# Performance work log

Hardware: AMD Instinct MI355X
Metric: run time of the kernel (lower is better)

The kernel has to match this reference:

```python
import jax, jax.numpy as jnp
import numpy as np
from jax import lax

EPS = 1e-5

def setup_inputs() -> dict:
    key = jax.random.key(0)
    ks = jax.random.split(key, 8)
    B, D, H, W = 2, 96, 96, 96
    K, N, R = 4, 16, 6
    return {
        "x": jax.random.normal(ks[0], (B, D, H, W), jnp.float32),
        "x_proj_weight": jax.random.normal(ks[1], (K, R + 2 * N, D), jnp.float32) * 0.05,
        "dt_projs_weight": jax.random.normal(ks[2], (K, D, R), jnp.float32) * 0.05,
        "dt_projs_bias": jax.random.normal(ks[3], (K, D), jnp.float32) * 0.05,
        "A_logs": jax.random.uniform(ks[4], (K * D, N), jnp.float32, 0.0, 1.0),
        "Ds": jax.random.normal(ks[5], (K * D,), jnp.float32) * 0.1,
        "norm_weight": jnp.ones((D,), jnp.float32),
        "norm_bias": jnp.zeros((D,), jnp.float32),
    }

def _cross_scan(x):
    # x: [B,C,H,W] -> xs: [B,4,C,L]; dirs: row-major, col-major, and their flips
    B, C, H, W = x.shape
    x_hw = x.reshape(B, C, H * W)
    x_wh = jnp.swapaxes(x, 2, 3).reshape(B, C, H * W)
    return jnp.stack([x_hw, x_wh, x_hw[..., ::-1], x_wh[..., ::-1]], axis=1)

def _cross_merge(ys, H, W):
    # ys: [B,4,C,L] -> y: [B,C,L]
    B, K, C, L = ys.shape
    ys = ys[:, 0:2] + ys[:, 2:4][..., ::-1]
    y_wh = jnp.swapaxes(ys[:, 1].reshape(B, C, W, H), 2, 3).reshape(B, C, L)
    return ys[:, 0] + y_wh

def _forward(x, x_proj_weight, dt_projs_weight, dt_projs_bias, A_logs, Ds,
             norm_weight, norm_bias):
    B, D, H, W = x.shape
    L = H * W
    K, _, R = dt_projs_weight.shape
    N = A_logs.shape[1]

    xs = _cross_scan(x)                                        # [B,K,D,L]
    x_dbl = jnp.einsum('bkdl,kcd->bkcl', xs, x_proj_weight)    # [B,K,R+2N,L]
    dts, Bs, Cs = x_dbl[:, :, :R], x_dbl[:, :, R:R + N], x_dbl[:, :, R + N:]
    dts = jnp.einsum('bkrl,kdr->bkdl', dts, dt_projs_weight)   # [B,K,D,L]

    A = -jnp.exp(A_logs).reshape(K, D, N)                      # [K,D,N]
    delta = jax.nn.softplus(dts + dt_projs_bias[None, :, :, None])  # [B,K,D,L]

    # time-major for scan
    u_t = jnp.moveaxis(xs, 3, 0)       # [L,B,K,D]
    d_t = jnp.moveaxis(delta, 3, 0)    # [L,B,K,D]
    B_t = jnp.moveaxis(Bs, 3, 0)       # [L,B,K,N]
    C_t = jnp.moveaxis(Cs, 3, 0)       # [L,B,K,N]

    def step(h, inp):
        u, dlt, b, c = inp
        h = jnp.exp(dlt[..., None] * A) * h + (dlt * u)[..., None] * b[:, :, None, :]
        y = jnp.einsum('bkdn,bkn->bkd', h, c)
        return h, y

    h0 = jnp.zeros((B, K, D, N), xs.dtype)
    _, ys = lax.scan(step, h0, (u_t, d_t, B_t, C_t))           # ys: [L,B,K,D]
    ys = jnp.moveaxis(ys, 0, 3)                                # [B,K,D,L]
    ys = ys + Ds.reshape(1, K, D, 1) * xs                      # skip term

    y = _cross_merge(ys, H, W)                                 # [B,D,L]
    y = jnp.swapaxes(y, 1, 2)                                  # [B,L,D]
    # out_norm: LayerNorm over channel dim
    mu = y.mean(-1, keepdims=True)
    var = y.var(-1, keepdims=True)
    y = (y - mu) / jnp.sqrt(var + EPS) * norm_weight + norm_bias
    return y.reshape(B, H, W, D)

def reference(x, x_proj_weight, dt_projs_weight, dt_projs_bias, A_logs, Ds,
              norm_weight, norm_bias):
    return _forward(x, x_proj_weight, dt_projs_weight, dt_projs_bias,
                    A_logs, Ds, norm_weight, norm_bias)
```

## Files before the change

kernel.cpp:

```cpp
#include <hip/hip_runtime.h>
#include <hip/hip_bf16.h>
#include <hip/hip_fp16.h>


constexpr int Bn = 2, Kn = 4, Dn = 96, Hn = 96, Wn = 96, Ln = Hn * Wn;
constexpr int Nn = 16, Rn = 6;
constexpr int CCn = 144, CLn = 64;

#define DI __device__ __forceinline__

typedef _Float16 half2v __attribute__((ext_vector_type(2)));

DI float bf2f(unsigned short u) { return __uint_as_float(((unsigned)u) << 16); }
DI bool probe_bf16(const void* nw) { return ((const unsigned*)nw)[0] == 0x3F803F80u; }
DI float ld_in(const void* p, long i, bool bf) {
  return bf ? bf2f(((const unsigned short*)p)[i]) : ((const float*)p)[i];
}
DI float fexp2(float x) {
#if __has_builtin(__builtin_amdgcn_exp2f)
  return __builtin_amdgcn_exp2f(x);
#else
  return exp2f(x);
#endif
}
DI float softplus_fast(float v) {
  return (v > 15.f) ? v : __logf(1.f + __expf(v));
}
DI float dot2acc(unsigned a, unsigned b, float c) {
#if __has_builtin(__builtin_amdgcn_fdot2)
  half2v av, bv;
  __builtin_memcpy(&av, &a, 4);
  __builtin_memcpy(&bv, &b, 4);
  return __builtin_amdgcn_fdot2(av, bv, c, false);
#else
  __half2 ah = *(__half2*)&a, bh = *(__half2*)&b;
  float2 af = __half22float2(ah), bf2_ = __half22float2(bh);
  return fmaf(af.y, bf2_.y, fmaf(af.x, bf2_.x, c));
#endif
}
DI float quad_reduce_add(float v) {
  int a = __builtin_amdgcn_mov_dpp(__float_as_int(v), 0xB1, 0xF, 0xF, true);
  v += __int_as_float(a);
  int b = __builtin_amdgcn_mov_dpp(__float_as_int(v), 0x4E, 0xF, 0xF, true);
  v += __int_as_float(b);
  return v;
}
constexpr float LOG2E = 1.44269504088896340736f;

__global__ __launch_bounds__(256) void k_prep(
    const void* __restrict__ x, const void* __restrict__ xpw,
    const void* __restrict__ dtw, const void* __restrict__ dtb,
    const void* __restrict__ Al, const void* __restrict__ Ds,
    const void* __restrict__ nw, const void* __restrict__ nb,
    float* __restrict__ xl, float* __restrict__ xlT,
    float* __restrict__ wp_f, float* __restrict__ wdt_f,
    float* __restrict__ bias_f, float* __restrict__ Al_f,
    float* __restrict__ dsum, float* __restrict__ nw_f, float* __restrict__ nb_f) {
  __shared__ float tile[96 * 97];
  bool bf = probe_bf16(nw);
  int h = blockIdx.x, b = blockIdx.y;
  int tid = threadIdx.x;
  int fi = (blockIdx.y * gridDim.x + blockIdx.x) * 256 + tid;
  int fgs = gridDim.x * gridDim.y * 256;
  for (int i = fi; i < Kn * 38 * Dn; i += fgs) wp_f[i] = ld_in(xpw, i, bf);
  for (int i = fi; i < Kn * Dn * Rn; i += fgs) wdt_f[i] = ld_in(dtw, i, bf);
  for (int i = fi; i < Kn * Dn; i += fgs) bias_f[i] = ld_in(dtb, i, bf);
  for (int i = fi; i < Kn * Dn * Nn; i += fgs)
    Al_f[i] = -__expf(ld_in(Al, i, bf)) * LOG2E;
  for (int i = fi; i < Dn; i += fgs) {
    dsum[i] = ld_in(Ds, i, bf) + ld_in(Ds, 96 + i, bf) +
              ld_in(Ds, 192 + i, bf) + ld_in(Ds, 288 + i, bf);
    nw_f[i] = ld_in(nw, i, bf);
    nb_f[i] = ld_in(nb, i, bf);
  }
  long srcbase = (long)b * Dn * Ln + (long)h * 96;
  for (int i = tid; i < 96 * 96; i += 256) {
    int d = i / 96, w = i - d * 96;
    tile[d * 97 + w] = ld_in(x, srcbase + (long)d * Ln + w, bf);
  }
  __syncthreads();
  float* xlb = xl + (size_t)b * Ln * 96;
  float* xTb = xlT + (size_t)b * Ln * 96;
  for (int i = tid; i < 96 * 96; i += 256) {
    int w = i / 96, d = i - w * 96;
    float v = tile[d * 97 + w];
    xlb[(size_t)(h * 96 + w) * 96 + d] = v;
    xTb[(size_t)(w * 96 + h) * 96 + d] = v;
  }
}

__global__ __launch_bounds__(256) void k_proj(
    const float* __restrict__ xl, const float* __restrict__ xlT,
    const float* __restrict__ wp_f, const float* __restrict__ wdt_f,
    const float* __restrict__ bias_f, const float* __restrict__ Al_f,
    __half2* __restrict__ ddu, __half* __restrict__ BCh,
    float* __restrict__ PSg) {
  constexpr int TL = 64;
  __shared__ __half xt[TL * 102];
  __shared__ __half wp[40 * 100];
  __shared__ __half xd2[TL * 40];
  __shared__ unsigned wdt_u[96 * 4];
  __shared__ float bias[96];
  int tile = blockIdx.x, k = blockIdx.y, b = blockIdx.z;
  int l0 = tile * TL;
  int tid = threadIdx.x;
  bool rev = (k & 2) != 0;

  for (int i = tid; i < 40 * 100; i += 256) {
    int c = i / 100, dd = i - c * 100;
    wp[i] = __float2half((c < 38 && dd < 96) ? wp_f[k * 38 * 96 + c * 96 + dd]
                                             : 0.f);
  }
  for (int i = tid; i < 96 * 3; i += 256) {
    int d = i / 3, rr = i - d * 3;
    __half2 hv = __floats2half2_rn(wdt_f[k * 576 + d * 6 + rr * 2],
                                   wdt_f[k * 576 + d * 6 + rr * 2 + 1]);
    wdt_u[d * 4 + rr] = *(unsigned*)&hv;
  }
  if (tid < 96) bias[tid] = bias_f[k * 96 + tid];
  {
    const float* xsrc = ((k & 1) ? xlT : xl) + (size_t)b * Ln * 96;
    for (int i = tid; i < TL * 24; i += 256) {
      int r = i / 24, q = i - r * 24;
      int g = rev ? (Ln - 1 - l0 - r) : (l0 + r);
      float4 v = *(const float4*)(xsrc + (size_t)g * 96 + q * 4);
      *(__half2*)(&xt[r * 102 + q * 4]) = __floats2half2_rn(v.x, v.y);
      *(__half2*)(&xt[r * 102 + q * 4 + 2]) = __floats2half2_rn(v.z, v.w);
    }
  }
  __syncthreads();

  {
    int jg = tid & 31, cg = tid >> 5;
    int j0 = jg * 2, c0 = cg * 5;
    float acc[5][2];
#pragma unroll
    for (int i = 0; i < 5; ++i) { acc[i][0] = 0.f; acc[i][1] = 0.f; }
    for (int dd = 0; dd < 96; dd += 4) {
      uint2 xa = *(const uint2*)&xt[(j0 + 0) * 102 + dd];
      uint2 xb = *(const uint2*)&xt[(j0 + 1) * 102 + dd];
#pragma unroll
      for (int i = 0; i < 5; ++i) {
        uint2 wv = *(const uint2*)&wp[(c0 + i) * 100 + dd];
        acc[i][0] = dot2acc(xa.x, wv.x, acc[i][0]);
        acc[i][0] = dot2acc(xa.y, wv.y, acc[i][0]);
        acc[i][1] = dot2acc(xb.x, wv.x, acc[i][1]);
        acc[i][1] = dot2acc(xb.y, wv.y, acc[i][1]);
      }
    }
#pragma unroll
    for (int i = 0; i < 5; ++i) {
      xd2[j0 * 40 + c0 + i] = __float2half(acc[i][0]);
      xd2[(j0 + 1) * 40 + c0 + i] = __float2half(acc[i][1]);
    }
  }
  __syncthreads();

  size_t bk = (size_t)b * 4 + k;
  {
    __half2* o = (__half2*)(BCh + (bk * (size_t)Ln + l0) * 32);
    for (int i = tid; i < TL * 16; i += 256) {
      int j = i >> 4, cp = i & 15;
      int c = cp * 2;
      int ng = c >> 3, idx = c & 7;
      int ch = (idx < 4) ? (6 + ng * 4 + idx) : (22 + ng * 4 + (idx - 4));
      o[i] = *(const __half2*)&xd2[j * 40 + ch];
    }
  }
  if (tid < 192) {
    int d = tid >> 1, hg = tid & 1;
    unsigned wv0 = wdt_u[d * 4], wv1 = wdt_u[d * 4 + 1], wv2 = wdt_u[d * 4 + 2];
    float bd = bias[d];
    float ac2[8];
    *(float4*)&ac2[0] = *(const float4*)&Al_f[(k * 96 + d) * 16 + hg * 8];
    *(float4*)&ac2[4] = *(const float4*)&Al_f[(k * 96 + d) * 16 + hg * 8 + 4];
    float P[8] = {1.f, 1.f, 1.f, 1.f, 1.f, 1.f, 1.f, 1.f};
    float S[8] = {0.f, 0.f, 0.f, 0.f, 0.f, 0.f, 0.f, 0.f};
    __half2* dcol = ddu + (bk * (size_t)Ln + l0) * 96 + d;
#pragma unroll 2
    for (int t = 0; t < TL; ++t) {
      uint2 xr01 = *(const uint2*)&xd2[t * 40];
      unsigned xr2 = *(const unsigned*)&xd2[t * 40 + 4];
      float v = dot2acc(xr01.x, wv0,
                dot2acc(xr01.y, wv1,
                dot2acc(xr2, wv2, bd)));
      float sp = softplus_fast(v);
      float u = __half2float(xt[t * 102 + d]);
      __half2 pk = __floats2half2_rn(sp, sp * u);
      if (hg == 0) dcol[(size_t)t * 96] = pk;
      float2 pf = __half22float2(pk);
      float spc = pf.x, fy = pf.y;
#pragma unroll
      for (int w = 0; w < 4; ++w) {
        unsigned bw = *(const unsigned*)&xd2[t * 40 + 6 + 8 * hg + 2 * w];
        float2 Bv = __half22float2(*(__half2*)&bw);
        float a0 = fexp2(spc * ac2[w * 2]);
        P[w * 2] *= a0;
        S[w * 2] = fmaf(a0, S[w * 2], fy * Bv.x);
        float a1 = fexp2(spc * ac2[w * 2 + 1]);
        P[w * 2 + 1] *= a1;
        S[w * 2 + 1] = fmaf(a1, S[w * 2 + 1], fy * Bv.y);
      }
    }
    size_t ob = ((size_t)(bk * 96 + d) * CCn + tile) * 32 + hg * 8;
    *(float4*)&PSg[ob] = make_float4(P[0], P[1], P[2], P[3]);
    *(float4*)&PSg[ob + 4] = make_float4(P[4], P[5], P[6], P[7]);
    *(float4*)&PSg[ob + 16] = make_float4(S[0], S[1], S[2], S[3]);
    *(float4*)&PSg[ob + 20] = make_float4(S[4], S[5], S[6], S[7]);
  }
}

__global__ __launch_bounds__(256) void k_midscan(float* __restrict__ PSg) {
  __shared__ float Pl[256], Sl[256];
  int bkd = blockIdx.x;
  int tid = threadIdx.x;
  int g = tid >> 4, n = tid & 15;
  constexpr int CPG = CCn / 16;
  size_t base = ((size_t)bkd * CCn + (size_t)g * CPG) * 32 + n;
  float Pr[CPG], Sr[CPG];
#pragma unroll
  for (int i = 0; i < CPG; ++i) {
    Pr[i] = PSg[base + (size_t)i * 32];
    Sr[i] = PSg[base + (size_t)i * 32 + 16];
  }
  float Pa = 1.f, Sa = 0.f;
#pragma unroll
  for (int i = 0; i < CPG; ++i) { Sa = fmaf(Pr[i], Sa, Sr[i]); Pa *= Pr[i]; }
  Pl[tid] = Pa;
  Sl[tid] = Sa;
  __syncthreads();
#pragma unroll
  for (int s = 1; s < 16; s <<= 1) {
    float Pp = 1.f, Sp = 0.f;
    if (g >= s) { Pp = Pl[(g - s) * 16 + n]; Sp = Sl[(g - s) * 16 + n]; }
    __syncthreads();
    if (g >= s) {
      Sl[tid] = fmaf(Pl[tid], Sp, Sl[tid]);
      Pl[tid] *= Pp;
    }
    __syncthreads();
  }
  float h = (g == 0) ? 0.f : Sl[(g - 1) * 16 + n];
#pragma unroll
  for (int i = 0; i < CPG; ++i) {
    PSg[base + (size_t)i * 32] = h;
    h = fmaf(Pr[i], h, Sr[i]);
  }
}

__global__ __launch_bounds__(192) void k_scan2(
    const __half2* __restrict__ ddu, const __half* __restrict__ BCh,
    const float* __restrict__ Al_f, const float* __restrict__ PSg,
    __half* __restrict__ ysH) {
  __shared__ __half2 dd_s[CLn * 96];
  __shared__ __half bc_s[CLn * 32];
  int chunk = blockIdx.x, k = blockIdx.y, b = blockIdx.z;
  int tid = threadIdx.x;
  int dp = tid >> 2, ng = tid & 3;
  int d0 = dp * 2, n0 = ng * 4;
  int bk = b * 4 + k;
  int t0 = chunk * CLn;
  float ac[2][4];
#pragma unroll
  for (int dd = 0; dd < 2; ++dd)
#pragma unroll
    for (int j = 0; j < 4; ++j)
      ac[dd][j] = Al_f[(k * 96 + d0 + dd) * 16 + n0 + j];
  {
    const uint4* dsrc = (const uint4*)(ddu + ((size_t)bk * Ln + t0) * 96);
    uint4* ddst = (uint4*)dd_s;
    for (int i = tid; i < CLn * 96 / 4; i += 192) ddst[i] = dsrc[i];
    const uint4* bsrc = (const uint4*)(BCh + ((size_t)bk * Ln + t0) * 32);
    uint4* bdst = (uint4*)bc_s;
    for (int i = tid; i < CLn * 32 * 2 / 16; i += 192) bdst[i] = bsrc[i];
  }
  float4 ha = *(const float4*)(PSg + ((size_t)(bk * 96 + d0) * CCn + chunk) * 32 + n0);
  float4 hb = *(const float4*)(PSg + ((size_t)(bk * 96 + d0 + 1) * CCn + chunk) * 32 + n0);
  float h[2][4] = {{ha.x, ha.y, ha.z, ha.w}, {hb.x, hb.y, hb.z, hb.w}};
  __syncthreads();

#pragma unroll 2
  for (int t = 0; t < CLn; ++t) {
    union { uint2 u; __half2 h2[2]; } dv;
    dv.u = *(const uint2*)&dd_s[t * 96 + d0];
    union { uint4 u; __half2 h2[4]; } bc;
    bc.u = *(const uint4*)&bc_s[t * 32 + ng * 8];
    float2 f0 = __half22float2(dv.h2[0]);
    float2 f1 = __half22float2(dv.h2[1]);
    float2 b01 = __half22float2(bc.h2[0]);
    float2 b23 = __half22float2(bc.h2[1]);
    float2 c01 = __half22float2(bc.h2[2]);
    float2 c23 = __half22float2(bc.h2[3]);
    float Ba[4] = {b01.x, b01.y, b23.x, b23.y};
    float Ca[4] = {c01.x, c01.y, c23.x, c23.y};
    float py0 = 0.f, py1 = 0.f;
#pragma unroll
    for (int j = 0; j < 4; ++j) {
      float a0 = fexp2(f0.x * ac[0][j]);
      h[0][j] = fmaf(a0, h[0][j], f0.y * Ba[j]);
      py0 = fmaf(h[0][j], Ca[j], py0);
      float a1 = fexp2(f1.x * ac[1][j]);
      h[1][j] = fmaf(a1, h[1][j], f1.y * Ba[j]);
      py1 = fmaf(h[1][j], Ca[j], py1);
    }
    py0 = quad_reduce_add(py0);
    py1 = quad_reduce_add(py1);
    if (ng == 0)
      *(__half2*)&ysH[((size_t)bk * Ln + t0 + t) * 96 + d0] =
          __halves2half2(__float2half(py0), __float2half(py1));
  }
}

__global__ __launch_bounds__(256) void k_merge_ln(
    const __half* __restrict__ ysH, const float* __restrict__ xl,
    const float* __restrict__ dsum, const void* __restrict__ nwraw,
    const float* __restrict__ nw_f, const float* __restrict__ nb_f,
    void* __restrict__ outv) {
  __shared__ float yt[64 * 98];
  __shared__ float nwf[96], nbf[96], dsm[96], mu_s[64], rs_s[64];
  bool bf = probe_bf16(nwraw);
  int tile = blockIdx.x, b = blockIdx.y;
  int h0 = (tile / 12) * 8, w0 = (tile % 12) * 8;
  int tid = threadIdx.x;
  if (tid < 96) {
    nwf[tid] = nw_f[tid];
    nbf[tid] = nb_f[tid];
    dsm[tid] = dsum[tid];
  }
  const __half* y0 = ysH + (size_t)(b * 4 + 0) * Ln * 96;
  const __half* y1 = ysH + (size_t)(b * 4 + 1) * Ln * 96;
  const __half* y2 = ysH + (size_t)(b * 4 + 2) * Ln * 96;
  const __half* y3 = ysH + (size_t)(b * 4 + 3) * Ln * 96;
  const float* xb = xl + (size_t)b * Ln * 96;
  __syncthreads();
  for (int i = tid; i < 64 * 48; i += 256) {
    int rr = i / 48, dp = i - rr * 48, d = dp * 2;
    int hh = h0 + (rr >> 3), ww = w0 + (rr & 7);
    int l = hh * 96 + ww, t1 = ww * 96 + hh;
    float2 v0 = __half22float2(*(const __half2*)&y0[(size_t)l * 96 + d]);
    float2 v1 = __half22float2(*(const __half2*)&y1[(size_t)t1 * 96 + d]);
    float2 v2 = __half22float2(*(const __half2*)&y2[(size_t)(Ln - 1 - l) * 96 + d]);
    float2 v3 = __half22float2(*(const __half2*)&y3[(size_t)(Ln - 1 - t1) * 96 + d]);
    float2 xv = *(const float2*)&xb[(size_t)l * 96 + d];
    float2 r;
    r.x = v0.x + v1.x + v2.x + v3.x + dsm[d] * xv.x;
    r.y = v0.y + v1.y + v2.y + v3.y + dsm[d + 1] * xv.y;
    *(float2*)&yt[rr * 98 + d] = r;
  }
  __syncthreads();
  {
    int rr = tid >> 2, qq = tid & 3;
    float s = 0.f, ss = 0.f;
#pragma unroll 4
    for (int d2 = 0; d2 < 24; ++d2) {
      float v = yt[rr * 98 + qq * 24 + d2];
      s += v;
      ss += v * v;
    }
    s = quad_reduce_add(s);
    ss = quad_reduce_add(ss);
    if (qq == 0) {
      float mu = s * (1.f / 96.f);
      float var = fmaxf(ss * (1.f / 96.f) - mu * mu, 0.f);
      mu_s[rr] = mu;
      rs_s[rr] = rsqrtf(var + 1e-5f);
    }
  }
  __syncthreads();
  for (int i = tid; i < 64 * 48; i += 256) {
    int rr = i / 48, dp = i - rr * 48, d = dp * 2;
    int hh = h0 + (rr >> 3), ww = w0 + (rr & 7);
    size_t idx = ((size_t)b * Ln + hh * 96 + ww) * 96 + d;
    float2 yv = *(const float2*)&yt[rr * 98 + d];
    float mu = mu_s[rr], rs = rs_s[rr];
    float o0 = (yv.x - mu) * rs * nwf[d] + nbf[d];
    float o1 = (yv.y - mu) * rs * nwf[d + 1] + nbf[d + 1];
    if (bf) {
      union { unsigned u; unsigned short us[2]; } pk;
      __hip_bfloat16 b0 = __float2bfloat16(o0), b1 = __float2bfloat16(o1);
      pk.us[0] = *(unsigned short*)&b0;
      pk.us[1] = *(unsigned short*)&b1;
      *(unsigned*)&((__hip_bfloat16*)outv)[idx] = pk.u;
    } else {
      *(float2*)&((float*)outv)[idx] = make_float2(o0, o1);
    }
  }
}

extern "C" void kernel_launch(void* const* d_in, const int* in_sizes, int n_in,
                              void* d_out, int out_size, void* d_ws, size_t ws_size,
                              hipStream_t stream) {
  const void* x   = d_in[0];
  const void* xpw = d_in[1];
  const void* dtw = d_in[2];
  const void* dtb = d_in[3];
  const void* Al  = d_in[4];
  const void* Ds  = d_in[5];
  const void* nw  = d_in[6];
  const void* nb  = d_in[7];

  char* ws = (char*)d_ws;
  size_t off = 0;
  auto alloc = [&](size_t bytes) {
    char* p = ws + off;
    off += (bytes + 511) & ~(size_t)511;
    return p;
  };
  float* xl    = (float*)alloc((size_t)Bn * Ln * Dn * 4);
  float* xlT   = (float*)alloc((size_t)Bn * Ln * Dn * 4);
  float* wp_f  = (float*)alloc((size_t)Kn * 38 * Dn * 4);
  float* wdt_f = (float*)alloc((size_t)Kn * Dn * Rn * 4);
  float* bias_f= (float*)alloc((size_t)Kn * Dn * 4);
  float* Al_f  = (float*)alloc((size_t)Kn * Dn * Nn * 4);
  float* dsum  = (float*)alloc((size_t)Dn * 4);
  float* nw_f  = (float*)alloc((size_t)Dn * 4);
  float* nb_f  = (float*)alloc((size_t)Dn * 4);
  __half2* ddu = (__half2*)alloc((size_t)Bn * Kn * Ln * Dn * 4);
  __half* BCh  = (__half*)alloc((size_t)Bn * Kn * Ln * 32 * 2);
  float* PS    = (float*)alloc((size_t)Bn * Kn * Dn * CCn * 32 * 4);
  __half* ysH  = (__half*)alloc((size_t)Bn * Kn * Ln * Dn * 2);
  (void)ws_size; (void)in_sizes; (void)n_in; (void)out_size;

  k_prep<<<dim3(Hn, Bn), dim3(256), 0, stream>>>(
      x, xpw, dtw, dtb, Al, Ds, nw, nb, xl, xlT, wp_f, wdt_f, bias_f, Al_f,
      dsum, nw_f, nb_f);
  k_proj<<<dim3(Ln / 64, Kn, Bn), dim3(256), 0, stream>>>(
      xl, xlT, wp_f, wdt_f, bias_f, Al_f, ddu, BCh, PS);
  k_midscan<<<dim3(Bn * Kn * Dn), dim3(256), 0, stream>>>(PS);
  k_scan2<<<dim3(CCn, Kn, Bn), dim3(192), 0, stream>>>(ddu, BCh, Al_f, PS, ysH);
  k_merge_ln<<<dim3(144, Bn), dim3(256), 0, stream>>>(ysH, xl, dsum, nw, nw_f,
                                                      nb_f, d_out);
}
```

Baseline: 198.7 us.

## Halve scan chunk length and pre-pack fp16 projection weights in prep kernel

Scan chunks shrink from 64 to 32 timesteps, which doubles the chunk count and the number of projection tiles, giving more parallel blocks in the projection and second-pass scan kernels. The projection weights are converted to padded fp16 and packed dt weights once in the prep kernel, so each projection block only does vectorized copies into shared memory instead of per-block conversion. In exchange the chunk-prefix buffer doubles, the mid-scan kernel has twice as many serial chunk-combine steps, and each projection thread now computes one row instead of two, which reduces weight reuse per shared-memory load.

```diff
diff --git a/kernel.cpp b/kernel.cpp
--- a/kernel.cpp
+++ b/kernel.cpp
@@ -5,7 +5,7 @@
 
 constexpr int Bn = 2, Kn = 4, Dn = 96, Hn = 96, Wn = 96, Ln = Hn * Wn;
 constexpr int Nn = 16, Rn = 6;
-constexpr int CCn = 144, CLn = 64;
+constexpr int CCn = 288, CLn = 32;
 
 #define DI __device__ __forceinline__
 
@@ -53,7 +53,7 @@
     const void* __restrict__ Al, const void* __restrict__ Ds,
     const void* __restrict__ nw, const void* __restrict__ nb,
     float* __restrict__ xl, float* __restrict__ xlT,
-    float* __restrict__ wp_f, float* __restrict__ wdt_f,
+    __half* __restrict__ wp_h, unsigned* __restrict__ wdt_p,
     float* __restrict__ bias_f, float* __restrict__ Al_f,
     float* __restrict__ dsum, float* __restrict__ nw_f, float* __restrict__ nb_f) {
   __shared__ float tile[96 * 97];
@@ -62,9 +62,29 @@
   int tid = threadIdx.x;
   int fi = (blockIdx.y * gridDim.x + blockIdx.x) * 256 + tid;
   int fgs = gridDim.x * gridDim.y * 256;
-  for (int i = fi; i < Kn * 38 * Dn; i += fgs) wp_f[i] = ld_in(xpw, i, bf);
-  for (int i = fi; i < Kn * Dn * Rn; i += fgs) wdt_f[i] = ld_in(dtw, i, bf);
-  for (int i = fi; i < Kn * Dn; i += fgs) bias_f[i] = ld_in(dtb, i, bf);
+  for (int i = fi; i < Kn * 4000; i += fgs) {
+    int k = i / 4000, r = i - k * 4000;
+    int c = r / 100, dd = r - c * 100;
+    wp_h[i] = __float2half(
+        (c < 38 && dd < 96) ? ld_in(xpw, (long)k * 38 * 96 + c * 96 + dd, bf)
+                            : 0.f);
+  }
+  for (int i = fi; i < Kn * Dn; i += fgs) {
+    float r01a = ld_in(dtw, (long)i * 6 + 0, bf);
+    float r01b = ld_in(dtw, (long)i * 6 + 1, bf);
+    float r23a = ld_in(dtw, (long)i * 6 + 2, bf);
+    float r23b = ld_in(dtw, (long)i * 6 + 3, bf);
+    float r45a = ld_in(dtw, (long)i * 6 + 4, bf);
+    float r45b = ld_in(dtw, (long)i * 6 + 5, bf);
+    __half2 h01 = __floats2half2_rn(r01a, r01b);
+    __half2 h23 = __floats2half2_rn(r23a, r23b);
+    __half2 h45 = __floats2half2_rn(r45a, r45b);
+    wdt_p[i * 4 + 0] = *(unsigned*)&h01;
+    wdt_p[i * 4 + 1] = *(unsigned*)&h23;
+    wdt_p[i * 4 + 2] = *(unsigned*)&h45;
+    wdt_p[i * 4 + 3] = 0u;
+    bias_f[i] = ld_in(dtb, i, bf);
+  }
   for (int i = fi; i < Kn * Dn * Nn; i += fgs)
     Al_f[i] = -__expf(ld_in(Al, i, bf)) * LOG2E;
   for (int i = fi; i < Dn; i += fgs) {
@@ -91,11 +111,11 @@
 
 __global__ __launch_bounds__(256) void k_proj(
     const float* __restrict__ xl, const float* __restrict__ xlT,
-    const float* __restrict__ wp_f, const float* __restrict__ wdt_f,
+    const __half* __restrict__ wp_h, const unsigned* __restrict__ wdt_p,
     const float* __restrict__ bias_f, const float* __restrict__ Al_f,
     __half2* __restrict__ ddu, __half* __restrict__ BCh,
     float* __restrict__ PSg) {
-  constexpr int TL = 64;
+  constexpr int TL = 32;
   __shared__ __half xt[TL * 102];
   __shared__ __half wp[40 * 100];
   __shared__ __half xd2[TL * 40];
@@ -106,18 +126,13 @@
   int tid = threadIdx.x;
   bool rev = (k & 2) != 0;
 
-  for (int i = tid; i < 40 * 100; i += 256) {
-    int c = i / 100, dd = i - c * 100;
-    wp[i] = __float2half((c < 38 && dd < 96) ? wp_f[k * 38 * 96 + c * 96 + dd]
-                                             : 0.f);
-  }
-  for (int i = tid; i < 96 * 3; i += 256) {
-    int d = i / 3, rr = i - d * 3;
-    __half2 hv = __floats2half2_rn(wdt_f[k * 576 + d * 6 + rr * 2],
-                                   wdt_f[k * 576 + d * 6 + rr * 2 + 1]);
-    wdt_u[d * 4 + rr] = *(unsigned*)&hv;
-  }
-  if (tid < 96) bias[tid] = bias_f[k * 96 + tid];
+  {
+    const uint4* wsrc = (const uint4*)(wp_h + (size_t)k * 4000);
+    for (int i = tid; i < 500; i += 256) ((uint4*)wp)[i] = wsrc[i];
+    const uint4* dsrc = (const uint4*)(wdt_p + (size_t)k * 384);
+    for (int i = tid; i < 96; i += 256) ((uint4*)wdt_u)[i] = dsrc[i];
+    if (tid < 96) bias[tid] = bias_f[k * 96 + tid];
+  }
   {
     const float* xsrc = ((k & 1) ? xlT : xl) + (size_t)b * Ln * 96;
     for (int i = tid; i < TL * 24; i += 256) {
@@ -132,27 +147,19 @@
 
   {
     int jg = tid & 31, cg = tid >> 5;
-    int j0 = jg * 2, c0 = cg * 5;
-    float acc[5][2];
-#pragma unroll
-    for (int i = 0; i < 5; ++i) { acc[i][0] = 0.f; acc[i][1] = 0.f; }
+    int c0 = cg * 5;
+    float acc[5] = {0.f, 0.f, 0.f, 0.f, 0.f};
     for (int dd = 0; dd < 96; dd += 4) {
-      uint2 xa = *(const uint2*)&xt[(j0 + 0) * 102 + dd];
-      uint2 xb = *(const uint2*)&xt[(j0 + 1) * 102 + dd];
+      uint2 xa = *(const uint2*)&xt[jg * 102 + dd];
 #pragma unroll
       for (int i = 0; i < 5; ++i) {
         uint2 wv = *(const uint2*)&wp[(c0 + i) * 100 + dd];
-        acc[i][0] = dot2acc(xa.x, wv.x, acc[i][0]);
-        acc[i][0] = dot2acc(xa.y, wv.y, acc[i][0]);
-        acc[i][1] = dot2acc(xb.x, wv.x, acc[i][1]);
-        acc[i][1] = dot2acc(xb.y, wv.y, acc[i][1]);
+        acc[i] = dot2acc(xa.x, wv.x, acc[i]);
+        acc[i] = dot2acc(xa.y, wv.y, acc[i]);
       }
     }
 #pragma unroll
-    for (int i = 0; i < 5; ++i) {
-      xd2[j0 * 40 + c0 + i] = __float2half(acc[i][0]);
-      xd2[(j0 + 1) * 40 + c0 + i] = __float2half(acc[i][1]);
-    }
+    for (int i = 0; i < 5; ++i) xd2[jg * 40 + c0 + i] = __float2half(acc[i]);
   }
   __syncthreads();
 
@@ -408,8 +415,8 @@
   };
   float* xl    = (float*)alloc((size_t)Bn * Ln * Dn * 4);
   float* xlT   = (float*)alloc((size_t)Bn * Ln * Dn * 4);
-  float* wp_f  = (float*)alloc((size_t)Kn * 38 * Dn * 4);
-  float* wdt_f = (float*)alloc((size_t)Kn * Dn * Rn * 4);
+  __half* wp_h = (__half*)alloc((size_t)Kn * 4000 * 2);
+  unsigned* wdt_p = (unsigned*)alloc((size_t)Kn * Dn * 4 * 4);
   float* bias_f= (float*)alloc((size_t)Kn * Dn * 4);
   float* Al_f  = (float*)alloc((size_t)Kn * Dn * Nn * 4);
   float* dsum  = (float*)alloc((size_t)Dn * 4);
@@ -422,10 +429,10 @@
   (void)ws_size; (void)in_sizes; (void)n_in; (void)out_size;
 
   k_prep<<<dim3(Hn, Bn), dim3(256), 0, stream>>>(
-      x, xpw, dtw, dtb, Al, Ds, nw, nb, xl, xlT, wp_f, wdt_f, bias_f, Al_f,
+      x, xpw, dtw, dtb, Al, Ds, nw, nb, xl, xlT, wp_h, wdt_p, bias_f, Al_f,
       dsum, nw_f, nb_f);
-  k_proj<<<dim3(Ln / 64, Kn, Bn), dim3(256), 0, stream>>>(
-      xl, xlT, wp_f, wdt_f, bias_f, Al_f, ddu, BCh, PS);
+  k_proj<<<dim3(Ln / 32, Kn, Bn), dim3(256), 0, stream>>>(
+      xl, xlT, wp_h, wdt_p, bias_f, Al_f, ddu, BCh, PS);
   k_midscan<<<dim3(Bn * Kn * Dn), dim3(256), 0, stream>>>(PS);
   k_scan2<<<dim3(CCn, Kn, Bn), dim3(192), 0, stream>>>(ddu, BCh, Al_f, PS, ysH);
   k_merge_ln<<<dim3(144, Bn), dim3(256), 0, stream>>>(ysH, xl, dsum, nw, nw_f,
```

After: 184.4 us. 1.08x faster.

## Fuse projection, chunk-carry scan and output scan into one cooperative kernel

Applied to the files above, without the earlier changes.

Merges k_proj, k_midscan and k_scan2 into a single cooperative kernel with grid-wide syncs. Projected B/C and delta stay in shared memory across the phases instead of round-tripping ddu/BCh through global memory. It also precomputes fp16 weights in k_prep and replaces the per-step P product with one exp2 of the summed delta. This adds dependence on a cooperative launch of 1152 blocks fitting co-resident (occupancy hint of 5), falls back to the split path if the launch fails, and pays for grid-sync overhead.

```diff
diff --git a/kernel.cpp b/kernel.cpp
--- a/kernel.cpp
+++ b/kernel.cpp
@@ -1,11 +1,14 @@
 #include <hip/hip_runtime.h>
 #include <hip/hip_bf16.h>
 #include <hip/hip_fp16.h>
-
+#include <hip/hip_cooperative_groups.h>
+
+
+namespace cg = cooperative_groups;
 
 constexpr int Bn = 2, Kn = 4, Dn = 96, Hn = 96, Wn = 96, Ln = Hn * Wn;
 constexpr int Nn = 16, Rn = 6;
-constexpr int CCn = 144, CLn = 64;
+constexpr int TLn = 64, CCn = 144, CLn = 64;
 
 #define DI __device__ __forceinline__
 
@@ -45,6 +48,10 @@
   v += __int_as_float(b);
   return v;
 }
+DI float pair_reduce_add(float v) {
+  int a = __builtin_amdgcn_mov_dpp(__float_as_int(v), 0xB1, 0xF, 0xF, true);
+  return v + __int_as_float(a);
+}
 constexpr float LOG2E = 1.44269504088896340736f;
 
 __global__ __launch_bounds__(256) void k_prep(
@@ -53,7 +60,7 @@
     const void* __restrict__ Al, const void* __restrict__ Ds,
     const void* __restrict__ nw, const void* __restrict__ nb,
     float* __restrict__ xl, float* __restrict__ xlT,
-    float* __restrict__ wp_f, float* __restrict__ wdt_f,
+    __half* __restrict__ wp_h, unsigned* __restrict__ wdt_p,
     float* __restrict__ bias_f, float* __restrict__ Al_f,
     float* __restrict__ dsum, float* __restrict__ nw_f, float* __restrict__ nb_f) {
   __shared__ float tile[96 * 97];
@@ -62,9 +69,24 @@
   int tid = threadIdx.x;
   int fi = (blockIdx.y * gridDim.x + blockIdx.x) * 256 + tid;
   int fgs = gridDim.x * gridDim.y * 256;
-  for (int i = fi; i < Kn * 38 * Dn; i += fgs) wp_f[i] = ld_in(xpw, i, bf);
-  for (int i = fi; i < Kn * Dn * Rn; i += fgs) wdt_f[i] = ld_in(dtw, i, bf);
-  for (int i = fi; i < Kn * Dn; i += fgs) bias_f[i] = ld_in(dtb, i, bf);
+  for (int i = fi; i < Kn * 3800; i += fgs) {
+    int k = i / 3800, r = i - k * 3800;
+    int c = r / 100, dd = r - c * 100;
+    wp_h[i] = __float2half(
+        (dd < 96) ? ld_in(xpw, (long)k * 38 * 96 + c * 96 + dd, bf) : 0.f);
+  }
+  for (int i = fi; i < Kn * Dn; i += fgs) {
+    __half2 h01 = __floats2half2_rn(ld_in(dtw, (long)i * 6 + 0, bf),
+                                    ld_in(dtw, (long)i * 6 + 1, bf));
+    __half2 h23 = __floats2half2_rn(ld_in(dtw, (long)i * 6 + 2, bf),
+                                    ld_in(dtw, (long)i * 6 + 3, bf));
+    __half2 h45 = __floats2half2_rn(ld_in(dtw, (long)i * 6 + 4, bf),
+                                    ld_in(dtw, (long)i * 6 + 5, bf));
+    wdt_p[i * 3 + 0] = *(unsigned*)&h01;
+    wdt_p[i * 3 + 1] = *(unsigned*)&h23;
+    wdt_p[i * 3 + 2] = *(unsigned*)&h45;
+    bias_f[i] = ld_in(dtb, i, bf);
+  }
   for (int i = fi; i < Kn * Dn * Nn; i += fgs)
     Al_f[i] = -__expf(ld_in(Al, i, bf)) * LOG2E;
   for (int i = fi; i < Dn; i += fgs) {
@@ -89,36 +111,28 @@
   }
 }
 
-__global__ __launch_bounds__(256) void k_proj(
-    const float* __restrict__ xl, const float* __restrict__ xlT,
-    const float* __restrict__ wp_f, const float* __restrict__ wdt_f,
-    const float* __restrict__ bias_f, const float* __restrict__ Al_f,
-    __half2* __restrict__ ddu, __half* __restrict__ BCh,
-    float* __restrict__ PSg) {
-  constexpr int TL = 64;
+template <bool COOP>
+DI void fused_body(const float* __restrict__ xl, const float* __restrict__ xlT,
+                   const __half* __restrict__ wp_h,
+                   const unsigned* __restrict__ wdt_p,
+                   const float* __restrict__ bias_f,
+                   const float* __restrict__ Al_f, float* __restrict__ PSg,
+                   __half* __restrict__ ysH, __half2* __restrict__ ddu,
+                   __half* __restrict__ BCh) {
+  constexpr int TL = TLn;
   __shared__ __half xt[TL * 102];
-  __shared__ __half wp[40 * 100];
+  __shared__ __half wpd[TL * 96];
   __shared__ __half xd2[TL * 40];
-  __shared__ unsigned wdt_u[96 * 4];
-  __shared__ float bias[96];
   int tile = blockIdx.x, k = blockIdx.y, b = blockIdx.z;
   int l0 = tile * TL;
   int tid = threadIdx.x;
+  int bk = b * 4 + k;
   bool rev = (k & 2) != 0;
 
-  for (int i = tid; i < 40 * 100; i += 256) {
-    int c = i / 100, dd = i - c * 100;
-    wp[i] = __float2half((c < 38 && dd < 96) ? wp_f[k * 38 * 96 + c * 96 + dd]
-                                             : 0.f);
-  }
-  for (int i = tid; i < 96 * 3; i += 256) {
-    int d = i / 3, rr = i - d * 3;
-    __half2 hv = __floats2half2_rn(wdt_f[k * 576 + d * 6 + rr * 2],
-                                   wdt_f[k * 576 + d * 6 + rr * 2 + 1]);
-    wdt_u[d * 4 + rr] = *(unsigned*)&hv;
-  }
-  if (tid < 96) bias[tid] = bias_f[k * 96 + tid];
   {
+    const uint4* wsrc = (const uint4*)(wp_h + (size_t)k * 3800);
+    for (int i = tid; i < 475; i += 256) ((uint4*)wpd)[i] = wsrc[i];
+    if (tid < 25) ((uint4*)wpd)[475 + tid] = make_uint4(0u, 0u, 0u, 0u);
     const float* xsrc = ((k & 1) ? xlT : xl) + (size_t)b * Ln * 96;
     for (int i = tid; i < TL * 24; i += 256) {
       int r = i / 24, q = i - r * 24;
@@ -141,7 +155,7 @@
       uint2 xb = *(const uint2*)&xt[(j0 + 1) * 102 + dd];
 #pragma unroll
       for (int i = 0; i < 5; ++i) {
-        uint2 wv = *(const uint2*)&wp[(c0 + i) * 100 + dd];
+        uint2 wv = *(const uint2*)&wpd[(c0 + i) * 100 + dd];
         acc[i][0] = dot2acc(xa.x, wv.x, acc[i][0]);
         acc[i][0] = dot2acc(xa.y, wv.y, acc[i][0]);
         acc[i][1] = dot2acc(xb.x, wv.x, acc[i][1]);
@@ -150,15 +164,17 @@
     }
 #pragma unroll
     for (int i = 0; i < 5; ++i) {
-      xd2[j0 * 40 + c0 + i] = __float2half(acc[i][0]);
-      xd2[(j0 + 1) * 40 + c0 + i] = __float2half(acc[i][1]);
-    }
-  }
-  __syncthreads();
-
-  size_t bk = (size_t)b * 4 + k;
-  {
-    __half2* o = (__half2*)(BCh + (bk * (size_t)Ln + l0) * 32);
+      if (c0 + i < 40) {
+        xd2[j0 * 40 + c0 + i] = __float2half(acc[i][0]);
+        xd2[(j0 + 1) * 40 + c0 + i] = __float2half(acc[i][1]);
+      }
+    }
+  }
+  __syncthreads();
+
+  size_t bk_l0 = (size_t)bk * Ln + l0;
+  if constexpr (!COOP) {
+    __half2* o = (__half2*)(BCh + bk_l0 * 32);
     for (int i = tid; i < TL * 16; i += 256) {
       int j = i >> 4, cp = i & 15;
       int c = cp * 2;
@@ -169,14 +185,16 @@
   }
   if (tid < 192) {
     int d = tid >> 1, hg = tid & 1;
-    unsigned wv0 = wdt_u[d * 4], wv1 = wdt_u[d * 4 + 1], wv2 = wdt_u[d * 4 + 2];
-    float bd = bias[d];
+    int kd = k * 96 + d;
+    unsigned wv0 = wdt_p[kd * 3], wv1 = wdt_p[kd * 3 + 1],
+             wv2 = wdt_p[kd * 3 + 2];
+    float bd = bias_f[kd];
     float ac2[8];
-    *(float4*)&ac2[0] = *(const float4*)&Al_f[(k * 96 + d) * 16 + hg * 8];
-    *(float4*)&ac2[4] = *(const float4*)&Al_f[(k * 96 + d) * 16 + hg * 8 + 4];
-    float P[8] = {1.f, 1.f, 1.f, 1.f, 1.f, 1.f, 1.f, 1.f};
+    *(float4*)&ac2[0] = *(const float4*)&Al_f[kd * 16 + hg * 8];
+    *(float4*)&ac2[4] = *(const float4*)&Al_f[kd * 16 + hg * 8 + 4];
+    float spsum = 0.f;
     float S[8] = {0.f, 0.f, 0.f, 0.f, 0.f, 0.f, 0.f, 0.f};
-    __half2* dcol = ddu + (bk * (size_t)Ln + l0) * 96 + d;
+    __half2* dcol = ddu + bk_l0 * 96 + d;
 #pragma unroll 2
     for (int t = 0; t < TL; ++t) {
       uint2 xr01 = *(const uint2*)&xd2[t * 40];
@@ -185,29 +203,152 @@
                 dot2acc(xr01.y, wv1,
                 dot2acc(xr2, wv2, bd)));
       float sp = softplus_fast(v);
+      __half sph = __float2half(sp);
+      float spc = __half2float(sph);
       float u = __half2float(xt[t * 102 + d]);
-      __half2 pk = __floats2half2_rn(sp, sp * u);
-      if (hg == 0) dcol[(size_t)t * 96] = pk;
-      float2 pf = __half22float2(pk);
-      float spc = pf.x, fy = pf.y;
+      __half fyh = __float2half(spc * u);
+      float fy = __half2float(fyh);
+      if (hg == 0) {
+        if constexpr (COOP) wpd[t * 96 + d] = sph;
+        else dcol[(size_t)t * 96] = __halves2half2(sph, fyh);
+      }
+      spsum += spc;
+      unsigned bw0 = *(const unsigned*)&xd2[t * 40 + 6 + hg * 8];
+      unsigned bw1 = *(const unsigned*)&xd2[t * 40 + 8 + hg * 8];
+      unsigned bw2 = *(const unsigned*)&xd2[t * 40 + 10 + hg * 8];
+      unsigned bw3 = *(const unsigned*)&xd2[t * 40 + 12 + hg * 8];
+      unsigned bws[4] = {bw0, bw1, bw2, bw3};
 #pragma unroll
       for (int w = 0; w < 4; ++w) {
-        unsigned bw = *(const unsigned*)&xd2[t * 40 + 6 + 8 * hg + 2 * w];
-        float2 Bv = __half22float2(*(__half2*)&bw);
+        float2 Bv = __half22float2(*(__half2*)&bws[w]);
         float a0 = fexp2(spc * ac2[w * 2]);
-        P[w * 2] *= a0;
         S[w * 2] = fmaf(a0, S[w * 2], fy * Bv.x);
         float a1 = fexp2(spc * ac2[w * 2 + 1]);
-        P[w * 2 + 1] *= a1;
         S[w * 2 + 1] = fmaf(a1, S[w * 2 + 1], fy * Bv.y);
       }
     }
+    float P[8];
+#pragma unroll
+    for (int j = 0; j < 8; ++j) P[j] = fexp2(spsum * ac2[j]);
     size_t ob = ((size_t)(bk * 96 + d) * CCn + tile) * 32 + hg * 8;
     *(float4*)&PSg[ob] = make_float4(P[0], P[1], P[2], P[3]);
     *(float4*)&PSg[ob + 4] = make_float4(P[4], P[5], P[6], P[7]);
     *(float4*)&PSg[ob + 16] = make_float4(S[0], S[1], S[2], S[3]);
     *(float4*)&PSg[ob + 20] = make_float4(S[4], S[5], S[6], S[7]);
   }
+
+  if constexpr (COOP) {
+    __threadfence();
+    cg::this_grid().sync();
+    __threadfence();
+    {
+      __shared__ float Pl[256], Sl[256];
+      int flatb =
+          (blockIdx.z * gridDim.y + blockIdx.y) * gridDim.x + blockIdx.x;
+      if (flatb < Bn * Kn * Dn) {
+        int bkd = flatb;
+        int g = tid >> 4, n = tid & 15;
+        constexpr int CPG = CCn / 16;
+        size_t base = ((size_t)bkd * CCn + (size_t)g * CPG) * 32 + n;
+        float Pr[CPG], Sr[CPG];
+#pragma unroll
+        for (int i = 0; i < CPG; ++i) {
+          Pr[i] = PSg[base + (size_t)i * 32];
+          Sr[i] = PSg[base + (size_t)i * 32 + 16];
+        }
+        float Pa = 1.f, Sa = 0.f;
+#pragma unroll
+        for (int i = 0; i < CPG; ++i) {
+          Sa = fmaf(Pr[i], Sa, Sr[i]);
+          Pa *= Pr[i];
+        }
+        Pl[tid] = Pa;
+        Sl[tid] = Sa;
+        __syncthreads();
+#pragma unroll
+        for (int s = 1; s < 16; s <<= 1) {
+          float Pp = 1.f, Sp = 0.f;
+          if (g >= s) { Pp = Pl[(g - s) * 16 + n]; Sp = Sl[(g - s) * 16 + n]; }
+          __syncthreads();
+          if (g >= s) {
+            Sl[tid] = fmaf(Pl[tid], Sp, Sl[tid]);
+            Pl[tid] *= Pp;
+          }
+          __syncthreads();
+        }
+        float hh = (g == 0) ? 0.f : Sl[(g - 1) * 16 + n];
+#pragma unroll
+        for (int i = 0; i < CPG; ++i) {
+          PSg[base + (size_t)i * 32] = hh;
+          hh = fmaf(Pr[i], hh, Sr[i]);
+        }
+      }
+    }
+    __threadfence();
+    cg::this_grid().sync();
+    __threadfence();
+
+    if (tid < 192) {
+      int d = tid >> 1, hg = tid & 1;
+      int kd = k * 96 + d;
+      float ac2[8];
+      *(float4*)&ac2[0] = *(const float4*)&Al_f[kd * 16 + hg * 8];
+      *(float4*)&ac2[4] = *(const float4*)&Al_f[kd * 16 + hg * 8 + 4];
+      size_t hb = ((size_t)(bk * 96 + d) * CCn + tile) * 32 + hg * 8;
+      float4 h03 = *(const float4*)&PSg[hb];
+      float4 h47 = *(const float4*)&PSg[hb + 4];
+      float h[8] = {h03.x, h03.y, h03.z, h03.w, h47.x, h47.y, h47.z, h47.w};
+      __half* yb = ysH + bk_l0 * 96 + d;
+#pragma unroll 2
+      for (int t = 0; t < TL; ++t) {
+        float spc = __half2float(wpd[t * 96 + d]);
+        float u = __half2float(xt[t * 102 + d]);
+        float fy = __half2float(__float2half(spc * u));
+        unsigned bw0 = *(const unsigned*)&xd2[t * 40 + 6 + hg * 8];
+        unsigned bw1 = *(const unsigned*)&xd2[t * 40 + 8 + hg * 8];
+        unsigned bw2 = *(const unsigned*)&xd2[t * 40 + 10 + hg * 8];
+        unsigned bw3 = *(const unsigned*)&xd2[t * 40 + 12 + hg * 8];
+        unsigned cw0 = *(const unsigned*)&xd2[t * 40 + 22 + hg * 8];
+        unsigned cw1 = *(const unsigned*)&xd2[t * 40 + 24 + hg * 8];
+        unsigned cw2 = *(const unsigned*)&xd2[t * 40 + 26 + hg * 8];
+        unsigned cw3 = *(const unsigned*)&xd2[t * 40 + 28 + hg * 8];
+        unsigned bws[4] = {bw0, bw1, bw2, bw3};
+        unsigned cws[4] = {cw0, cw1, cw2, cw3};
+        float py = 0.f;
+#pragma unroll
+        for (int w = 0; w < 4; ++w) {
+          float2 Bv = __half22float2(*(__half2*)&bws[w]);
+          float2 Cv = __half22float2(*(__half2*)&cws[w]);
+          float a0 = fexp2(spc * ac2[w * 2]);
+          h[w * 2] = fmaf(a0, h[w * 2], fy * Bv.x);
+          py = fmaf(h[w * 2], Cv.x, py);
+          float a1 = fexp2(spc * ac2[w * 2 + 1]);
+          h[w * 2 + 1] = fmaf(a1, h[w * 2 + 1], fy * Bv.y);
+          py = fmaf(h[w * 2 + 1], Cv.y, py);
+        }
+        py = pair_reduce_add(py);
+        if (hg == 0) yb[(size_t)t * 96] = __float2half(py);
+      }
+    }
+  }
+}
+
+__global__ __launch_bounds__(256, 5) void k_fused_coop(
+    const float* __restrict__ xl, const float* __restrict__ xlT,
+    const __half* __restrict__ wp_h, const unsigned* __restrict__ wdt_p,
+    const float* __restrict__ bias_f, const float* __restrict__ Al_f,
+    float* __restrict__ PSg, __half* __restrict__ ysH,
+    __half2* __restrict__ ddu, __half* __restrict__ BCh) {
+  fused_body<true>(xl, xlT, wp_h, wdt_p, bias_f, Al_f, PSg, ysH, ddu, BCh);
+}
+
+__global__ __launch_bounds__(256, 5) void k_fused_split(
+    const float* __restrict__ xl, const float* __restrict__ xlT,
+    const __half* __restrict__ wp_h, const unsigned* __restrict__ wdt_p,
+    const float* __restrict__ bias_f, const float* __restrict__ Al_f,
+    float* __restrict__ PSg, __half* __restrict__ ysH,
+    __half2* __restrict__ ddu, __half* __restrict__ BCh) {
+  fused_body<false>(xl, xlT, wp_h, wdt_p, bias_f, Al_f, PSg, ysH, ddu, BCh);
 }
 
 __global__ __launch_bounds__(256) void k_midscan(float* __restrict__ PSg) {
@@ -408,26 +549,49 @@
   };
   float* xl    = (float*)alloc((size_t)Bn * Ln * Dn * 4);
   float* xlT   = (float*)alloc((size_t)Bn * Ln * Dn * 4);
-  float* wp_f  = (float*)alloc((size_t)Kn * 38 * Dn * 4);
-  float* wdt_f = (float*)alloc((size_t)Kn * Dn * Rn * 4);
+  __half* wp_h = (__half*)alloc((size_t)Kn * 3800 * 2);
+  unsigned* wdt_p = (unsigned*)alloc((size_t)Kn * Dn * 3 * 4);
   float* bias_f= (float*)alloc((size_t)Kn * Dn * 4);
   float* Al_f  = (float*)alloc((size_t)Kn * Dn * Nn * 4);
   float* dsum  = (float*)alloc((size_t)Dn * 4);
   float* nw_f  = (float*)alloc((size_t)Dn * 4);
   float* nb_f  = (float*)alloc((size_t)Dn * 4);
+  float* PS    = (float*)alloc((size_t)Bn * Kn * Dn * CCn * 32 * 4);
+  __half* ysH  = (__half*)alloc((size_t)Bn * Kn * Ln * Dn * 2);
   __half2* ddu = (__half2*)alloc((size_t)Bn * Kn * Ln * Dn * 4);
   __half* BCh  = (__half*)alloc((size_t)Bn * Kn * Ln * 32 * 2);
-  float* PS    = (float*)alloc((size_t)Bn * Kn * Dn * CCn * 32 * 4);
-  __half* ysH  = (__half*)alloc((size_t)Bn * Kn * Ln * Dn * 2);
   (void)ws_size; (void)in_sizes; (void)n_in; (void)out_size;
 
   k_prep<<<dim3(Hn, Bn), dim3(256), 0, stream>>>(
-      x, xpw, dtw, dtb, Al, Ds, nw, nb, xl, xlT, wp_f, wdt_f, bias_f, Al_f,
+      x, xpw, dtw, dtb, Al, Ds, nw, nb, xl, xlT, wp_h, wdt_p, bias_f, Al_f,
       dsum, nw_f, nb_f);
-  k_proj<<<dim3(Ln / 64, Kn, Bn), dim3(256), 0, stream>>>(
-      xl, xlT, wp_f, wdt_f, bias_f, Al_f, ddu, BCh, PS);
-  k_midscan<<<dim3(Bn * Kn * Dn), dim3(256), 0, stream>>>(PS);
-  k_scan2<<<dim3(CCn, Kn, Bn), dim3(192), 0, stream>>>(ddu, BCh, Al_f, PS, ysH);
+
+  static int coop_ok = -1;
+  bool try_coop = (coop_ok != 0);
+  bool did_coop = false;
+  if (try_coop) {
+    const float* xl_c = xl; const float* xlT_c = xlT;
+    const __half* wp_c = wp_h; const unsigned* wdt_c = wdt_p;
+    const float* bias_c = bias_f; const float* Al_c = Al_f;
+    float* PS_c = PS; __half* ys_c = ysH; __half2* ddu_c = ddu;
+    __half* BC_c = BCh;
+    void* kargs[] = {(void*)&xl_c, (void*)&xlT_c, (void*)&wp_c, (void*)&wdt_c,
+                     (void*)&bias_c, (void*)&Al_c, (void*)&PS_c, (void*)&ys_c,
+                     (void*)&ddu_c, (void*)&BC_c};
+    hipError_t ce = hipLaunchCooperativeKernel(
+        (const void*)k_fused_coop, dim3(Ln / TLn, Kn, Bn), dim3(256), kargs,
+        0, stream);
+    did_coop = (ce == hipSuccess);
+    if (coop_ok == -1) coop_ok = did_coop ? 1 : 0;
+  }
+  if (!did_coop) {
+    k_fused_split<<<dim3(Ln / TLn, Kn, Bn), dim3(256), 0, stream>>>(
+        xl, xlT, wp_h, wdt_p, bias_f, Al_f, PS, ysH, ddu, BCh);
+    k_midscan<<<dim3(Bn * Kn * Dn), dim3(256), 0, stream>>>(PS);
+    k_scan2<<<dim3(CCn, Kn, Bn), dim3(192), 0, stream>>>(ddu, BCh, Al_f, PS,
+                                                         ysH);
+  }
+
   k_merge_ln<<<dim3(144, Bn), dim3(256), 0, stream>>>(ysH, xl, dsum, nw, nw_f,
                                                       nb_f, d_out);
 }
```

New measurement: 193.4 us. -2.7%, faster.
